# Kernel optimization log

Hardware: AMD Instinct MI355X
Metric: run time of the kernel (lower is better)

## Reference

```python
import jax, jax.numpy as jnp
import numpy as np

INVALID_TOKEN_ID = -1
B, K, V = 128, 8, 128000  # batch, spec length, vocab


def setup_inputs() -> dict:
    key = jax.random.key(0)
    k1, k2 = jax.random.split(key)
    draft_token_ids = jax.random.randint(k1, (B, K), 0, V, dtype=jnp.int64 if jax.config.jax_enable_x64 else jnp.int32)
    # target probs over vocab for B*(K+1) sampled positions
    target_probs = jax.random.uniform(k2, (B * (K + 1), V), dtype=jnp.float32)
    return {"draft_token_ids": draft_token_ids, "target_probs": target_probs}


def reference(draft_token_ids, target_probs):
    b, k = draft_token_ids.shape
    # greedy target tokens: argmax over vocab, reshaped to [B, K+1]
    output_token_ids = jnp.argmax(target_probs, axis=-1).reshape(b, k + 1).astype(draft_token_ids.dtype)
    # accept draft tokens while they match target greedy tokens (prefix match)
    accept_mask = jnp.cumprod((output_token_ids[:, :-1] == draft_token_ids).astype(jnp.int32), axis=1)
    valid_mask = output_token_ids != INVALID_TOKEN_ID
    generate_mask = jnp.concatenate(
        [accept_mask.astype(bool), jnp.zeros((b, 1), dtype=bool)], axis=1
    ) & valid_mask
    # first rejected position also emits the (bonus/corrected) target token
    zeros_mask = ~generate_mask
    first_zero_idx = jnp.argmax(zeros_mask.astype(jnp.float32), axis=1)
    rows_with_zero = jnp.any(zeros_mask, axis=1)
    fix = (jnp.arange(k + 1)[None, :] == first_zero_idx[:, None]) & rows_with_zero[:, None]
    generate_mask = generate_mask | fix
    return jnp.where(generate_mask, output_token_ids, INVALID_TOKEN_ID)
```

## Files before the change

### kernel.cpp

```cpp
#include <hip/hip_runtime.h>
#include <math.h>

#define INVALID_TOKEN_ID (-1)
constexpr int BB = 128;
constexpr int KK = 8;
constexpr int VV = 128000;
constexpr int ROWS = BB * (KK + 1);
constexpr int THREADS = 256;

__global__ __launch_bounds__(THREADS) void argmax_rows_kernel(
    const float* __restrict__ probs, int* __restrict__ amax_out) {
    const int row = blockIdx.x;
    const int tid = threadIdx.x;
    const float4* __restrict__ p4 =
        (const float4*)(probs + (size_t)row * VV);

    float best = -INFINITY;
    int bestIdx = VV;

    #pragma unroll 5
    for (int i = tid; i < VV / 4; i += THREADS) {
        float4 v = p4[i];
        int base = i * 4;
        if (v.x > best) { best = v.x; bestIdx = base; }
        if (v.y > best) { best = v.y; bestIdx = base + 1; }
        if (v.z > best) { best = v.z; bestIdx = base + 2; }
        if (v.w > best) { best = v.w; bestIdx = base + 3; }
    }

    #pragma unroll
    for (int off = 32; off > 0; off >>= 1) {
        float ov = __shfl_down(best, off, 64);
        int   oi = __shfl_down(bestIdx, off, 64);
        if (ov > best || (ov == best && oi < bestIdx)) {
            best = ov;
            bestIdx = oi;
        }
    }

    __shared__ float s_v[THREADS / 64];
    __shared__ int   s_i[THREADS / 64];
    const int wave = tid >> 6;
    const int lane = tid & 63;
    if (lane == 0) {
        s_v[wave] = best;
        s_i[wave] = bestIdx;
    }
    __syncthreads();
    if (tid == 0) {
        #pragma unroll
        for (int w = 1; w < THREADS / 64; ++w) {
            if (s_v[w] > best || (s_v[w] == best && s_i[w] < bestIdx)) {
                best = s_v[w];
                bestIdx = s_i[w];
            }
        }
        amax_out[row] = bestIdx;
    }
}

__global__ __launch_bounds__(128) void finalize_kernel(
    const int* __restrict__ draft, const int* __restrict__ amax,
    int* __restrict__ out) {
    const int b = threadIdx.x;
    if (b >= BB) return;
    const int* arow = amax + b * (KK + 1);
    const int* drow = draft + b * KK;
    int r = 0;
    while (r < KK && arow[r] == drow[r]) ++r;
    int* orow = out + b * (KK + 1);
    #pragma unroll
    for (int j = 0; j <= KK; ++j) {
        orow[j] = (j <= r) ? arow[j] : INVALID_TOKEN_ID;
    }
}

extern "C" void kernel_launch(void* const* d_in, const int* in_sizes, int n_in,
                              void* d_out, int out_size, void* d_ws, size_t ws_size,
                              hipStream_t stream) {
    const int*   draft = (const int*)d_in[0];
    const float* probs = (const float*)d_in[1];
    int* out  = (int*)d_out;
    int* amax = (int*)d_ws;

    argmax_rows_kernel<<<ROWS, THREADS, 0, stream>>>(probs, amax);
    finalize_kernel<<<1, 128, 0, stream>>>(draft, amax, out);
}
```

Before: 749.1 us.

## Fuse finalize into argmax kernel via per-batch atomic ticket counters

Removes the separate finalize launch: the last block to finish for each batch row, found through an atomic counter, runs the prefix-match and writes the output. The counters are zeroed with a memset each call. The argmax loop now uses 384 threads and keeps two independent running maxima per thread to raise loads in flight. Risks include the extra memset launch, atomic overhead, and a different block size for a memory-bound reduction.

```diff
diff --git a/kernel.cpp b/kernel.cpp
--- a/kernel.cpp
+++ b/kernel.cpp
@@ -6,35 +6,58 @@
 constexpr int KK = 8;
 constexpr int VV = 128000;
 constexpr int ROWS = BB * (KK + 1);
-constexpr int THREADS = 256;
+constexpr int THREADS = 384;
+constexpr int NV4 = VV / 4;
 
-__global__ __launch_bounds__(THREADS) void argmax_rows_kernel(
-    const float* __restrict__ probs, int* __restrict__ amax_out) {
+__global__ __launch_bounds__(THREADS) void rejsample_fused_kernel(
+    const float* __restrict__ probs,
+    const int* __restrict__ draft,
+    int* __restrict__ amax,
+    int* __restrict__ counters,
+    int* __restrict__ out) {
     const int row = blockIdx.x;
     const int tid = threadIdx.x;
-    const float4* __restrict__ p4 =
-        (const float4*)(probs + (size_t)row * VV);
+    const float4* __restrict__ p4 = (const float4*)(probs + (size_t)row * VV);
 
-    float best = -INFINITY;
-    int bestIdx = VV;
+    float bestA = -INFINITY, bestB = -INFINITY;
+    int idxA = VV, idxB = VV;
 
-    #pragma unroll 5
-    for (int i = tid; i < VV / 4; i += THREADS) {
-        float4 v = p4[i];
-        int base = i * 4;
-        if (v.x > best) { best = v.x; bestIdx = base; }
-        if (v.y > best) { best = v.y; bestIdx = base + 1; }
-        if (v.z > best) { best = v.z; bestIdx = base + 2; }
-        if (v.w > best) { best = v.w; bestIdx = base + 3; }
+    int i = tid;
+    #pragma unroll 2
+    for (; i + THREADS < NV4; i += 2 * THREADS) {
+        float4 va = p4[i];
+        float4 vb = p4[i + THREADS];
+        int ba = i * 4;
+        int bb = (i + THREADS) * 4;
+        if (va.x > bestA) { bestA = va.x; idxA = ba; }
+        if (va.y > bestA) { bestA = va.y; idxA = ba + 1; }
+        if (va.z > bestA) { bestA = va.z; idxA = ba + 2; }
+        if (va.w > bestA) { bestA = va.w; idxA = ba + 3; }
+        if (vb.x > bestB) { bestB = vb.x; idxB = bb; }
+        if (vb.y > bestB) { bestB = vb.y; idxB = bb + 1; }
+        if (vb.z > bestB) { bestB = vb.z; idxB = bb + 2; }
+        if (vb.w > bestB) { bestB = vb.w; idxB = bb + 3; }
+    }
+    if (i < NV4) {
+        float4 va = p4[i];
+        int ba = i * 4;
+        if (va.x > bestA) { bestA = va.x; idxA = ba; }
+        if (va.y > bestA) { bestA = va.y; idxA = ba + 1; }
+        if (va.z > bestA) { bestA = va.z; idxA = ba + 2; }
+        if (va.w > bestA) { bestA = va.w; idxA = ba + 3; }
+    }
+    if (bestB > bestA || (bestB == bestA && idxB < idxA)) {
+        bestA = bestB;
+        idxA = idxB;
     }
 
     #pragma unroll
     for (int off = 32; off > 0; off >>= 1) {
-        float ov = __shfl_down(best, off, 64);
-        int   oi = __shfl_down(bestIdx, off, 64);
-        if (ov > best || (ov == best && oi < bestIdx)) {
-            best = ov;
-            bestIdx = oi;
+        float ov = __shfl_down(bestA, off, 64);
+        int   oi = __shfl_down(idxA, off, 64);
+        if (ov > bestA || (ov == bestA && oi < idxA)) {
+            bestA = ov;
+            idxA = oi;
         }
     }
 
@@ -43,35 +66,39 @@
     const int wave = tid >> 6;
     const int lane = tid & 63;
     if (lane == 0) {
-        s_v[wave] = best;
-        s_i[wave] = bestIdx;
+        s_v[wave] = bestA;
+        s_i[wave] = idxA;
     }
     __syncthreads();
+
     if (tid == 0) {
         #pragma unroll
         for (int w = 1; w < THREADS / 64; ++w) {
-            if (s_v[w] > best || (s_v[w] == best && s_i[w] < bestIdx)) {
-                best = s_v[w];
-                bestIdx = s_i[w];
+            if (s_v[w] > bestA || (s_v[w] == bestA && s_i[w] < idxA)) {
+                bestA = s_v[w];
+                idxA = s_i[w];
             }
         }
-        amax_out[row] = bestIdx;
-    }
-}
-
-__global__ __launch_bounds__(128) void finalize_kernel(
-    const int* __restrict__ draft, const int* __restrict__ amax,
-    int* __restrict__ out) {
-    const int b = threadIdx.x;
-    if (b >= BB) return;
-    const int* arow = amax + b * (KK + 1);
-    const int* drow = draft + b * KK;
-    int r = 0;
-    while (r < KK && arow[r] == drow[r]) ++r;
-    int* orow = out + b * (KK + 1);
-    #pragma unroll
-    for (int j = 0; j <= KK; ++j) {
-        orow[j] = (j <= r) ? arow[j] : INVALID_TOKEN_ID;
+        const int b = row / (KK + 1);
+        __hip_atomic_store(&amax[row], idxA, __ATOMIC_RELEASE,
+                           __HIP_MEMORY_SCOPE_AGENT);
+        int ticket = __hip_atomic_fetch_add(&counters[b], 1, __ATOMIC_ACQ_REL,
+                                            __HIP_MEMORY_SCOPE_AGENT);
+        if (ticket == KK) {
+            int a[KK + 1];
+            #pragma unroll
+            for (int j = 0; j <= KK; ++j) {
+                a[j] = __hip_atomic_load(&amax[b * (KK + 1) + j],
+                                         __ATOMIC_ACQUIRE,
+                                         __HIP_MEMORY_SCOPE_AGENT);
+            }
+            int r = 0;
+            while (r < KK && a[r] == draft[b * KK + r]) ++r;
+            #pragma unroll
+            for (int j = 0; j <= KK; ++j) {
+                out[b * (KK + 1) + j] = (j <= r) ? a[j] : INVALID_TOKEN_ID;
+            }
+        }
     }
 }
 
@@ -80,9 +107,11 @@
                               hipStream_t stream) {
     const int*   draft = (const int*)d_in[0];
     const float* probs = (const float*)d_in[1];
-    int* out  = (int*)d_out;
-    int* amax = (int*)d_ws;
+    int* out      = (int*)d_out;
+    int* amax     = (int*)d_ws;
+    int* counters = amax + ROWS;
 
-    argmax_rows_kernel<<<ROWS, THREADS, 0, stream>>>(probs, amax);
-    finalize_kernel<<<1, 128, 0, stream>>>(draft, amax, out);
+    hipMemsetAsync(counters, 0, BB * sizeof(int), stream);
+    rejsample_fused_kernel<<<ROWS, THREADS, 0, stream>>>(probs, draft, amax,
+                                                         counters, out);
 }
```

New measurement: 862.4 us. 15.1% more time.
